# Performance work log

Hardware: AMD Instinct MI355X
Metric: run time of the kernel (lower is better)

The kernel has to match this reference:

```python
import jax, jax.numpy as jnp
import numpy as np
import math


def gelu_tanh(x):
    # BERT/GPT tanh-approx gelu, matching the torch source exactly
    c = math.sqrt(2.0 / math.pi)
    return 0.5 * x * (1.0 + jnp.tanh(c * (x + 0.044715 * x * x * x)))


def setup_inputs() -> dict:
    key = jax.random.key(0)
    k1, k2, k3, k4 = jax.random.split(key, 4)
    B, S, H, M = 8, 4096, 1024, 256
    hidden_sates = jax.random.normal(k1, (B, S, H), dtype=jnp.float32)
    token_type_ids = jax.random.randint(k2, (B, S), 0, M, dtype=jnp.int64)
    W = jax.random.normal(k3, (H, H), dtype=jnp.float32) * 0.02
    b = jax.random.normal(k4, (H,), dtype=jnp.float32) * 0.02
    return {"hidden_sates": hidden_sates, "token_type_ids": token_type_ids,
            "W": W, "b": b, "max_length": 256}


def reference(hidden_sates, token_type_ids, W, b, max_length):
    # hidden_sates: [B,S,H], token_type_ids: [B,S] in [0, max_length)
    B, S, H = hidden_sates.shape
    bidx = jnp.arange(B)[:, None]                      # [B,1], broadcasts vs [B,S]
    # segment-sum per batch row (equivalent to one_hot_from @ hidden_sates)
    cell_hidden = jnp.zeros((B, max_length, H), dtype=hidden_sates.dtype)
    cell_hidden = cell_hidden.at[bidx, token_type_ids].add(hidden_sates)  # [B,M,H]
    # nn.Linear: x @ W.T + b, then gelu
    cell_hidden = gelu_tanh(jnp.einsum('bmh,oh->bmo', cell_hidden, W) + b)
    # scatter back to sequence (equivalent to one_hot_to @ cell_hidden)
    seq_hidden = cell_hidden[bidx, token_type_ids]     # [B,S,H]
    return seq_hidden
```

## Files before the change

kernel.cpp:

```cpp
#include <hip/hip_runtime.h>
#include <hip/hip_bf16.h>
#include <math.h>

#define B_ 8
#define S_ 4096
#define H_ 1024
#define M_ 256
#define R_ (B_*M_)

typedef __attribute__((ext_vector_type(8))) short short8;
typedef __attribute__((ext_vector_type(4))) float f32x4;

__device__ __forceinline__ unsigned short f2bf(float x) {
  union { float f; unsigned int u; } v; v.f = x;
  unsigned int r = v.u + 0x7FFF + ((v.u >> 16) & 1);
  return (unsigned short)(r >> 16);
}
__device__ __forceinline__ float bf2f(unsigned short h) {
  union { unsigned int u; float f; } v; v.u = ((unsigned int)h) << 16;
  return v.f;
}
__device__ __forceinline__ int get_id(const void* tt, int is64, int idx) {
  return is64 ? (int)((const long long*)tt)[idx] : ((const int*)tt)[idx];
}

__global__ __launch_bounds__(256) void wconv_detect(const float* __restrict__ W,
                                                    const unsigned int* __restrict__ tt32,
                                                    unsigned short* __restrict__ whi,
                                                    unsigned short* __restrict__ wlo,
                                                    int* __restrict__ flag) {
  if (blockIdx.x == 0 && threadIdx.x < 64) {
    unsigned long long any = __ballot(tt32[threadIdx.x * 2 + 1] != 0u);
    if (threadIdx.x == 0) *flag = (any == 0ull) ? 1 : 0;
  }
  int i = blockIdx.x * 256 + threadIdx.x;
  float4 v = reinterpret_cast<const float4*>(W)[i];
  ushort4 hi, lo;
  hi.x = f2bf(v.x); lo.x = f2bf(v.x - bf2f(hi.x));
  hi.y = f2bf(v.y); lo.y = f2bf(v.y - bf2f(hi.y));
  hi.z = f2bf(v.z); lo.z = f2bf(v.z - bf2f(hi.z));
  hi.w = f2bf(v.w); lo.w = f2bf(v.w - bf2f(hi.w));
  reinterpret_cast<ushort4*>(whi)[i] = hi;
  reinterpret_cast<ushort4*>(wlo)[i] = lo;
}

__global__ __launch_bounds__(256) void seg_sum(const float* __restrict__ hidden,
                                               const void* __restrict__ tt,
                                               const int* __restrict__ flag,
                                               unsigned short* __restrict__ chi,
                                               unsigned short* __restrict__ clo) {
  const int bm = blockIdx.x;
  const int b  = bm >> 8;
  const int m  = bm & (M_ - 1);
  __shared__ int list[S_];
  __shared__ int cnt;
  const int t = threadIdx.x;
  if (t == 0) cnt = 0;
  __syncthreads();
  const int is64 = *flag;
  const int base = b * S_;
  #pragma unroll
  for (int c = 0; c < S_ / 256; ++c) {
    int s = c * 256 + t;
    if (get_id(tt, is64, base + s) == m) { int p = atomicAdd(&cnt, 1); list[p] = s; }
  }
  __syncthreads();
  const int n = cnt;
  float ax = 0.f, ay = 0.f, az = 0.f, aw = 0.f;
  const float4* hb = reinterpret_cast<const float4*>(hidden + (size_t)b * S_ * H_);
  for (int i = 0; i < n; ++i) {
    const int s = list[i];
    float4 v = hb[(size_t)s * (H_ / 4) + t];
    ax += v.x; ay += v.y; az += v.z; aw += v.w;
  }
  ushort4 hi, lo;
  hi.x = f2bf(ax); lo.x = f2bf(ax - bf2f(hi.x));
  hi.y = f2bf(ay); lo.y = f2bf(ay - bf2f(hi.y));
  hi.z = f2bf(az); lo.z = f2bf(az - bf2f(hi.z));
  hi.w = f2bf(aw); lo.w = f2bf(aw - bf2f(hi.w));
  *reinterpret_cast<ushort4*>(chi + (size_t)bm * H_ + t * 4) = hi;
  *reinterpret_cast<ushort4*>(clo + (size_t)bm * H_ + t * 4) = lo;
}

__global__ __launch_bounds__(256) void gemm_gelu(const unsigned short* __restrict__ Ahi,
                                                 const unsigned short* __restrict__ Alo,
                                                 const unsigned short* __restrict__ Bhi,
                                                 const unsigned short* __restrict__ Blo,
                                                 const float* __restrict__ bias,
                                                 float* __restrict__ C) {
  const int lane = threadIdx.x & 63;
  const int wid  = threadIdx.x >> 6;
  const int wm = wid >> 1, wn = wid & 1;
  const int rowBase = blockIdx.x * 64 + wm * 32;
  const int colBase = blockIdx.y * 128 + wn * 64;
  const int lr = lane & 15;
  const int kg = lane >> 4;

  f32x4 acc[2][4];
  #pragma unroll
  for (int mi = 0; mi < 2; ++mi)
    #pragma unroll
    for (int ni = 0; ni < 4; ++ni)
      acc[mi][ni] = (f32x4){0.f, 0.f, 0.f, 0.f};

  for (int k0 = 0; k0 < H_; k0 += 32) {
    short8 ah[2], al[2], bh[4], bl[4];
    #pragma unroll
    for (int mi = 0; mi < 2; ++mi) {
      const size_t off = (size_t)(rowBase + mi * 16 + lr) * H_ + k0 + kg * 8;
      ah[mi] = *reinterpret_cast<const short8*>(Ahi + off);
      al[mi] = *reinterpret_cast<const short8*>(Alo + off);
    }
    #pragma unroll
    for (int ni = 0; ni < 4; ++ni) {
      const size_t off = (size_t)(colBase + ni * 16 + lr) * H_ + k0 + kg * 8;
      bh[ni] = *reinterpret_cast<const short8*>(Bhi + off);
      bl[ni] = *reinterpret_cast<const short8*>(Blo + off);
    }
    #pragma unroll
    for (int mi = 0; mi < 2; ++mi)
      #pragma unroll
      for (int ni = 0; ni < 4; ++ni) {
        acc[mi][ni] = __builtin_amdgcn_mfma_f32_16x16x32_bf16(ah[mi], bh[ni], acc[mi][ni], 0, 0, 0);
        acc[mi][ni] = __builtin_amdgcn_mfma_f32_16x16x32_bf16(ah[mi], bl[ni], acc[mi][ni], 0, 0, 0);
        acc[mi][ni] = __builtin_amdgcn_mfma_f32_16x16x32_bf16(al[mi], bh[ni], acc[mi][ni], 0, 0, 0);
      }
  }

  const float cg = 0.7978845608028654f;
  #pragma unroll
  for (int mi = 0; mi < 2; ++mi) {
    #pragma unroll
    for (int ni = 0; ni < 4; ++ni) {
      const int col = colBase + ni * 16 + lr;
      const float bv = bias[col];
      #pragma unroll
      for (int j = 0; j < 4; ++j) {
        const int row = rowBase + mi * 16 + kg * 4 + j;
        float x = acc[mi][ni][j] + bv;
        float g = 0.5f * x * (1.0f + tanhf(cg * (x + 0.044715f * x * x * x)));
        C[(size_t)row * H_ + col] = g;
      }
    }
  }
}

__global__ __launch_bounds__(256) void gather_rows(const float* __restrict__ cell2,
                                                   const void* __restrict__ tt,
                                                   const int* __restrict__ flag,
                                                   float* __restrict__ out) {
  __shared__ int ids[8];
  const int r0 = blockIdx.x * 8;
  const int t  = threadIdx.x;
  if (t < 8) ids[t] = get_id(tt, *flag, r0 + t);
  __syncthreads();
  const int b = r0 >> 12;
  #pragma unroll
  for (int j = 0; j < 8; ++j) {
    const float4* src = reinterpret_cast<const float4*>(cell2 + (size_t)(b * M_ + ids[j]) * H_);
    float4* dst = reinterpret_cast<float4*>(out + (size_t)(r0 + j) * H_);
    dst[t] = src[t];
  }
}

extern "C" void kernel_launch(void* const* d_in, const int* in_sizes, int n_in,
                              void* d_out, int out_size, void* d_ws, size_t ws_size,
                              hipStream_t stream) {
  const float* hidden = (const float*)d_in[0];
  const void*  tt     = d_in[1];
  const float* W      = (const float*)d_in[2];
  const float* bias   = (const float*)d_in[3];
  float* out = (float*)d_out;

  char* ws = (char*)d_ws;
  int* flag = (int*)ws;
  unsigned short* chi = (unsigned short*)(ws + 256);
  unsigned short* clo = chi + (size_t)R_ * H_;
  unsigned short* whi = clo + (size_t)R_ * H_;
  unsigned short* wlo = whi + (size_t)H_ * H_;
  float*          cell2 = (float*)(wlo + (size_t)H_ * H_);

  wconv_detect<<<dim3(H_ * H_ / 1024), dim3(256), 0, stream>>>(W, (const unsigned int*)tt, whi, wlo, flag);
  seg_sum<<<dim3(R_), dim3(256), 0, stream>>>(hidden, tt, flag, chi, clo);
  gemm_gelu<<<dim3(R_ / 64, H_ / 128), dim3(256), 0, stream>>>(chi, clo, whi, wlo, bias, cell2);
  gather_rows<<<dim3(B_ * S_ / 8), dim3(256), 0, stream>>>(cell2, tt, flag, out);
}
```

Measured before the change: 313.3 us.

## Fuse GEMM+GELU with scatter-back to sequence via shared-memory tile

The gather kernel is merged into the GEMM epilogue. Each block computes a 64x128 GELU tile into LDS, then scans its batch's token ids for rows in its 64-cell range and writes the matching tile rows directly to the output. This removes the intermediate cell2 buffer round trip and one launch. Blocks now use 512 threads with smaller per-wave tiles. The cost is that every block rescans all 4096 token ids and uses about 50KB of LDS, which may limit occupancy.

```diff
diff --git a/kernel.cpp b/kernel.cpp
--- a/kernel.cpp
+++ b/kernel.cpp
@@ -82,45 +82,51 @@
   *reinterpret_cast<ushort4*>(clo + (size_t)bm * H_ + t * 4) = lo;
 }
 
-__global__ __launch_bounds__(256) void gemm_gelu(const unsigned short* __restrict__ Ahi,
-                                                 const unsigned short* __restrict__ Alo,
-                                                 const unsigned short* __restrict__ Bhi,
-                                                 const unsigned short* __restrict__ Blo,
-                                                 const float* __restrict__ bias,
-                                                 float* __restrict__ C) {
+__global__ __launch_bounds__(512) void gemm_gelu_scatter(
+    const unsigned short* __restrict__ Ahi, const unsigned short* __restrict__ Alo,
+    const unsigned short* __restrict__ Bhi, const unsigned short* __restrict__ Blo,
+    const float* __restrict__ bias, const void* __restrict__ tt,
+    const int* __restrict__ flag, float* __restrict__ out) {
   const int lane = threadIdx.x & 63;
   const int wid  = threadIdx.x >> 6;
-  const int wm = wid >> 1, wn = wid & 1;
-  const int rowBase = blockIdx.x * 64 + wm * 32;
-  const int colBase = blockIdx.y * 128 + wn * 64;
+  const int wm = wid >> 2, wn = wid & 3;
+  const int rowBase = blockIdx.x * 64;
+  const int b  = rowBase >> 8;
+  const int m0 = rowBase & (M_ - 1);
+  const int colBase = blockIdx.y * 128;
   const int lr = lane & 15;
   const int kg = lane >> 4;
 
-  f32x4 acc[2][4];
+  __shared__ float tile[64 * 132];
+  __shared__ int   list[S_];
+  __shared__ int   cnt;
+  if (threadIdx.x == 0) cnt = 0;
+
+  f32x4 acc[2][2];
   #pragma unroll
   for (int mi = 0; mi < 2; ++mi)
     #pragma unroll
-    for (int ni = 0; ni < 4; ++ni)
+    for (int ni = 0; ni < 2; ++ni)
       acc[mi][ni] = (f32x4){0.f, 0.f, 0.f, 0.f};
 
   for (int k0 = 0; k0 < H_; k0 += 32) {
-    short8 ah[2], al[2], bh[4], bl[4];
+    short8 ah[2], al[2], bh[2], bl[2];
     #pragma unroll
     for (int mi = 0; mi < 2; ++mi) {
-      const size_t off = (size_t)(rowBase + mi * 16 + lr) * H_ + k0 + kg * 8;
+      const size_t off = (size_t)(rowBase + wm * 32 + mi * 16 + lr) * H_ + k0 + kg * 8;
       ah[mi] = *reinterpret_cast<const short8*>(Ahi + off);
       al[mi] = *reinterpret_cast<const short8*>(Alo + off);
     }
     #pragma unroll
-    for (int ni = 0; ni < 4; ++ni) {
-      const size_t off = (size_t)(colBase + ni * 16 + lr) * H_ + k0 + kg * 8;
+    for (int ni = 0; ni < 2; ++ni) {
+      const size_t off = (size_t)(colBase + wn * 32 + ni * 16 + lr) * H_ + k0 + kg * 8;
       bh[ni] = *reinterpret_cast<const short8*>(Bhi + off);
       bl[ni] = *reinterpret_cast<const short8*>(Blo + off);
     }
     #pragma unroll
     for (int mi = 0; mi < 2; ++mi)
       #pragma unroll
-      for (int ni = 0; ni < 4; ++ni) {
+      for (int ni = 0; ni < 2; ++ni) {
         acc[mi][ni] = __builtin_amdgcn_mfma_f32_16x16x32_bf16(ah[mi], bh[ni], acc[mi][ni], 0, 0, 0);
         acc[mi][ni] = __builtin_amdgcn_mfma_f32_16x16x32_bf16(ah[mi], bl[ni], acc[mi][ni], 0, 0, 0);
         acc[mi][ni] = __builtin_amdgcn_mfma_f32_16x16x32_bf16(al[mi], bh[ni], acc[mi][ni], 0, 0, 0);
@@ -131,35 +137,41 @@
   #pragma unroll
   for (int mi = 0; mi < 2; ++mi) {
     #pragma unroll
-    for (int ni = 0; ni < 4; ++ni) {
-      const int col = colBase + ni * 16 + lr;
-      const float bv = bias[col];
+    for (int ni = 0; ni < 2; ++ni) {
+      const int col = wn * 32 + ni * 16 + lr;
+      const float bv = bias[colBase + col];
       #pragma unroll
       for (int j = 0; j < 4; ++j) {
-        const int row = rowBase + mi * 16 + kg * 4 + j;
+        const int row = wm * 32 + mi * 16 + kg * 4 + j;
         float x = acc[mi][ni][j] + bv;
-        float g = 0.5f * x * (1.0f + tanhf(cg * (x + 0.044715f * x * x * x)));
-        C[(size_t)row * H_ + col] = g;
+        tile[row * 132 + col] = 0.5f * x * (1.0f + tanhf(cg * (x + 0.044715f * x * x * x)));
       }
     }
   }
-}
+  __syncthreads();
 
-__global__ __launch_bounds__(256) void gather_rows(const float* __restrict__ cell2,
-                                                   const void* __restrict__ tt,
-                                                   const int* __restrict__ flag,
-                                                   float* __restrict__ out) {
-  __shared__ int ids[8];
-  const int r0 = blockIdx.x * 8;
-  const int t  = threadIdx.x;
-  if (t < 8) ids[t] = get_id(tt, *flag, r0 + t);
+  const int is64 = *flag;
+  const int base = b * S_;
+  #pragma unroll
+  for (int c = 0; c < S_ / 512; ++c) {
+    const int s = c * 512 + threadIdx.x;
+    const int id = get_id(tt, is64, base + s);
+    if ((id & ~63) == m0) { int p = atomicAdd(&cnt, 1); list[p] = (s << 6) | (id & 63); }
+  }
   __syncthreads();
-  const int b = r0 >> 12;
-  #pragma unroll
-  for (int j = 0; j < 8; ++j) {
-    const float4* src = reinterpret_cast<const float4*>(cell2 + (size_t)(b * M_ + ids[j]) * H_);
-    float4* dst = reinterpret_cast<float4*>(out + (size_t)(r0 + j) * H_);
-    dst[t] = src[t];
+
+  const int n = cnt;
+  const int half = lane >> 5;
+  const int q    = lane & 31;
+  for (int i0 = wid * 2; i0 < n; i0 += 16) {
+    const int ei = i0 + half;
+    if (ei < n) {
+      const int e = list[ei];
+      const int mloc = e & 63;
+      const int s = e >> 6;
+      float4 v = *reinterpret_cast<const float4*>(&tile[mloc * 132 + q * 4]);
+      *reinterpret_cast<float4*>(out + (size_t)(base + s) * H_ + colBase + q * 4) = v;
+    }
   }
 }
 
@@ -178,10 +190,8 @@
   unsigned short* clo = chi + (size_t)R_ * H_;
   unsigned short* whi = clo + (size_t)R_ * H_;
   unsigned short* wlo = whi + (size_t)H_ * H_;
-  float*          cell2 = (float*)(wlo + (size_t)H_ * H_);
 
   wconv_detect<<<dim3(H_ * H_ / 1024), dim3(256), 0, stream>>>(W, (const unsigned int*)tt, whi, wlo, flag);
   seg_sum<<<dim3(R_), dim3(256), 0, stream>>>(hidden, tt, flag, chi, clo);
-  gemm_gelu<<<dim3(R_ / 64, H_ / 128), dim3(256), 0, stream>>>(chi, clo, whi, wlo, bias, cell2);
-  gather_rows<<<dim3(B_ * S_ / 8), dim3(256), 0, stream>>>(cell2, tt, flag, out);
+  gemm_gelu_scatter<<<dim3(R_ / 64, H_ / 128), dim3(512), 0, stream>>>(chi, clo, whi, wlo, bias, tt, flag, out);
 }
```

New measurement: 320.3 us. +2.2%, slower.
